# Performance work log

Hardware: AMD Instinct MI355X
Metric: run time of the kernel (lower is better)

Reference implementation:

```python
import jax, jax.numpy as jnp
import numpy as np

HARMONICS = 5


def _harmonic_basis(x):
    k = jnp.arange(1, HARMONICS + 1, dtype=x.dtype)            # [H]
    kx = x[..., None] * k                                       # [B, D, H]
    sc = jnp.stack([jnp.sin(kx), jnp.cos(kx)], axis=-1)         # [B, D, H, 2]
    sc = sc.reshape(*x.shape, 2 * HARMONICS)                    # interleaved sin/cos
    ones = jnp.ones((*x.shape, 1), dtype=x.dtype)
    return jnp.concatenate([ones, sc], axis=-1)                 # [B, D, 2H+1]


def setup_inputs() -> dict:
    key = jax.random.key(0)
    k1, k2, k3 = jax.random.split(key, 3)
    B, D, F, H = 16384, 256, 11, 256
    x = jax.random.normal(k1, (B, D), dtype=jnp.float32)
    W = jax.random.normal(k2, (D, F, H), dtype=jnp.float32) * (1.0 / np.sqrt(F))
    b = jax.random.normal(k3, (D, H), dtype=jnp.float32) * 0.01
    return {"x": x, "W": W, "b": b}


def reference(x, W, b) -> jnp.ndarray:
    # basis expansion per feature, batched small GEMM, summed over features
    basis = _harmonic_basis(x)                                  # [B, D, F]
    out = jnp.einsum('bdf,dfh->bh', basis, W)                   # sum over features fused
    out = out + jnp.sum(b, axis=0)                              # sum of per-feature biases
    return out
```

## Files before the change

kernel.cpp:

```cpp
#include <hip/hip_runtime.h>
#include <hip/hip_bf16.h>
#include <hip/hip_fp16.h>


#define BDIM 16384
#define DDIM 256
#define HOUT 256
#define NKT  80
#define BM 128
#define BN 128

typedef _Float16 halfx8 __attribute__((ext_vector_type(8)));
typedef float floatx4 __attribute__((ext_vector_type(4)));

__device__ __forceinline__ unsigned short f2h(float f) {
    union { _Float16 h; unsigned short u; } v;
    v.h = (_Float16)f;
    return v.u;
}

#define INV2PI 0.15915494309189535f

__device__ __forceinline__ void hwsincos(float x, float* s, float* c) {
    const float r = x * INV2PI;
    float sv, cv;
    asm("v_sin_f32 %0, %1" : "=v"(sv) : "v"(r));
    asm("v_cos_f32 %0, %1" : "=v"(cv) : "v"(r));
    *s = sv; *c = cv;
}

__global__ void prep_kernel(const float* __restrict__ W, const float* __restrict__ bias,
                            unsigned short* __restrict__ Wfrag, float* __restrict__ c_part) {
    const int bid = blockIdx.x;
    const int t = threadIdx.x;
    if (bid < 4 * NKT) {
        const int kt = bid >> 2;
        const int sub = bid & 3;
        const int dtile = kt / 10;
        const int f = kt - dtile * 10 + 1;
        const int d0 = dtile * 32 + sub * 8;
        const float* wsrc = W + ((size_t)d0 * 11 + f) * 256 + t;
        union { unsigned short s[8]; int4 v; } buf;
#pragma unroll
        for (int dd = 0; dd < 8; ++dd)
            buf.s[dd] = f2h(wsrc[(size_t)dd * 11 * 256]);
        *(int4*)(Wfrag + ((size_t)kt * 256 + t) * 32 + sub * 8) = buf.v;
    } else {
        const int p = bid - 4 * NKT;
        float acc = 0.f;
#pragma unroll
        for (int dd = 0; dd < 32; ++dd) {
            const int d = p * 32 + dd;
            acc += W[(size_t)(d * 11) * 256 + t] + bias[(size_t)d * 256 + t];
        }
        c_part[p * 256 + t] = acc;
    }
}

__global__ __launch_bounds__(512, 2)
void kan_gemm(const float* __restrict__ x, const unsigned short* __restrict__ Wfrag,
              const float* __restrict__ c_part, float* __restrict__ out) {
    __shared__ unsigned short Bs[6][2 * 8 * 512];

    const int t = threadIdx.x;
    const int m0 = blockIdx.x * BM;
    const int h0 = blockIdx.y * BN;

    const int lane = t & 63;
    const int wave = t >> 6;
    const int wr = wave >> 1;
    const int wc = wave & 1;
    const int l15 = lane & 15;
    const int koff = lane >> 4;

    floatx4 acc[2][4];
#pragma unroll
    for (int i = 0; i < 2; ++i)
#pragma unroll
        for (int j = 0; j < 4; ++j)
            acc[i][j] = (floatx4){0.f, 0.f, 0.f, 0.f};

    const float* xr0 = x + (size_t)(m0 + wr * 32 + l15) * DDIM + koff * 8;

    float4 xn[4];
    xn[0] = *(const float4*)(xr0 + 0);
    xn[1] = *(const float4*)(xr0 + 4);
    xn[2] = *(const float4*)(xr0 + 16 * DDIM + 0);
    xn[3] = *(const float4*)(xr0 + 16 * DDIM + 4);

#pragma unroll
    for (int p = 0; p < 3; ++p) {
#pragma unroll
        for (int s = 0; s < 2; ++s) {
            const int c = wave * 2 + s;
            const int ktl = c >> 3;
            const int f = c & 7;
            const unsigned short* g = Wfrag + (size_t)(p * 2 + ktl) * 8192
                                    + (h0 + f * 16 + l15) * 32 + koff * 8;
            __builtin_amdgcn_global_load_lds((const void*)g,
                (void*)(&Bs[p][0] + c * 512), 16, 0, 0);
        }
    }

    __half2 s1h[8], c1h[8], skh[8], ckh[8];

#pragma unroll 1
    for (int dt = 0; dt < 8; ++dt) {
#pragma unroll
        for (int q = 0; q < 5; ++q) {

            if (q == 2) {
                const int dn = (dt < 7) ? dt + 1 : 7;
                xn[0] = *(const float4*)(xr0 + dn * 32 + 0);
                xn[1] = *(const float4*)(xr0 + dn * 32 + 4);
                xn[2] = *(const float4*)(xr0 + 16 * DDIM + dn * 32 + 0);
                xn[3] = *(const float4*)(xr0 + 16 * DDIM + dn * 32 + 4);
            }

            {
                int pt = dt * 5 + q + 3;
                if (pt > 39) pt = 39;
#pragma unroll
                for (int s = 0; s < 2; ++s) {
                    const int c = wave * 2 + s;
                    const int ktl = c >> 3;
                    const int f = c & 7;
                    const unsigned short* g = Wfrag + (size_t)(pt * 2 + ktl) * 8192
                                            + (h0 + f * 16 + l15) * 32 + koff * 8;
                    __builtin_amdgcn_global_load_lds((const void*)g,
                        (void*)(&Bs[(q + 3) % 5][0] + c * 512), 16, 0, 0);
                }
            }

            __builtin_amdgcn_sched_barrier(0);
            if (q == 2 || q == 3) {
                asm volatile("s_waitcnt vmcnt(10)" ::: "memory");
            } else {
                asm volatile("s_waitcnt vmcnt(6)" ::: "memory");
            }
            __builtin_amdgcn_s_barrier();
            __builtin_amdgcn_sched_barrier(0);

            if (q == 0) {
                const float xv[16] = {xn[0].x, xn[0].y, xn[0].z, xn[0].w,
                                      xn[1].x, xn[1].y, xn[1].z, xn[1].w,
                                      xn[2].x, xn[2].y, xn[2].z, xn[2].w,
                                      xn[3].x, xn[3].y, xn[3].z, xn[3].w};
#pragma unroll
                for (int p = 0; p < 8; ++p) {
                    float s0, c0, s1, c1;
                    hwsincos(xv[2 * p], &s0, &c0);
                    hwsincos(xv[2 * p + 1], &s1, &c1);
                    const __half2 sh = __floats2half2_rn(s0, s1);
                    const __half2 ch = __floats2half2_rn(c0, c1);
                    s1h[p] = sh; c1h[p] = ch;
                    skh[p] = sh; ckh[p] = ch;
                }
            }

#pragma unroll
            for (int s = 0; s < 2; ++s) {
                union { __half2 h2[4]; halfx8 v; } a0, a1;
                if (s == 0) {
#pragma unroll
                    for (int p = 0; p < 4; ++p) { a0.h2[p] = skh[p]; a1.h2[p] = skh[p + 4]; }
                } else {
#pragma unroll
                    for (int p = 0; p < 4; ++p) { a0.h2[p] = ckh[p]; a1.h2[p] = ckh[p + 4]; }
                }

                const unsigned short* fb = &Bs[q][(s * 8 + wc * 4) * 512 + lane * 8];
                const halfx8 b0 = *(const halfx8*)(fb);
                const halfx8 b1 = *(const halfx8*)(fb + 512);
                const halfx8 b2 = *(const halfx8*)(fb + 1024);
                const halfx8 b3 = *(const halfx8*)(fb + 1536);

                acc[0][0] = __builtin_amdgcn_mfma_f32_16x16x32_f16(a0.v, b0, acc[0][0], 0, 0, 0);
                acc[1][0] = __builtin_amdgcn_mfma_f32_16x16x32_f16(a1.v, b0, acc[1][0], 0, 0, 0);
                acc[0][1] = __builtin_amdgcn_mfma_f32_16x16x32_f16(a0.v, b1, acc[0][1], 0, 0, 0);
                acc[1][1] = __builtin_amdgcn_mfma_f32_16x16x32_f16(a1.v, b1, acc[1][1], 0, 0, 0);
                acc[0][2] = __builtin_amdgcn_mfma_f32_16x16x32_f16(a0.v, b2, acc[0][2], 0, 0, 0);
                acc[1][2] = __builtin_amdgcn_mfma_f32_16x16x32_f16(a1.v, b2, acc[1][2], 0, 0, 0);
                acc[0][3] = __builtin_amdgcn_mfma_f32_16x16x32_f16(a0.v, b3, acc[0][3], 0, 0, 0);
                acc[1][3] = __builtin_amdgcn_mfma_f32_16x16x32_f16(a1.v, b3, acc[1][3], 0, 0, 0);

                if (s == 1 && q < 4) {
#pragma unroll
                    for (int p = 0; p < 8; ++p) {
                        const __half2 t0 = __hmul2(ckh[p], s1h[p]);
                        const __half2 t1 = __hmul2(skh[p], s1h[p]);
                        const __half2 ns = __hfma2(skh[p], c1h[p], t0);
                        const __half2 nc = __hfma2(ckh[p], c1h[p], __hneg2(t1));
                        skh[p] = ns;
                        ckh[p] = nc;
                    }
                }
            }
        }
    }

    asm volatile("s_waitcnt vmcnt(0)" ::: "memory");

    float cj[4];
#pragma unroll
    for (int j = 0; j < 4; ++j) {
        const int col = h0 + wc * 64 + j * 16 + l15;
        float s = 0.f;
#pragma unroll
        for (int q = 0; q < 8; ++q) s += c_part[q * 256 + col];
        cj[j] = s;
    }
#pragma unroll
    for (int i = 0; i < 2; ++i) {
        const int row0 = m0 + wr * 32 + i * 16 + koff * 4;
#pragma unroll
        for (int j = 0; j < 4; ++j) {
            const int col = h0 + wc * 64 + j * 16 + l15;
#pragma unroll
            for (int r = 0; r < 4; ++r)
                out[(size_t)(row0 + r) * HOUT + col] = acc[i][j][r] + cj[j];
        }
    }
}

extern "C" void kernel_launch(void* const* d_in, const int* in_sizes, int n_in,
                              void* d_out, int out_size, void* d_ws, size_t ws_size,
                              hipStream_t stream) {
    const float* x = (const float*)d_in[0];
    const float* W = (const float*)d_in[1];
    const float* b = (const float*)d_in[2];
    float* out = (float*)d_out;

    unsigned short* Wfrag = (unsigned short*)d_ws;
    float* c_part = (float*)((char*)d_ws + (size_t)NKT * 256 * 32 * 2);

    prep_kernel<<<4 * NKT + 8, 256, 0, stream>>>(W, b, Wfrag, c_part);
    kan_gemm<<<dim3(BDIM / BM, HOUT / BN), 512, 0, stream>>>(x, Wfrag, c_part, out);
}
```

Measured before the change: 97.24 us.

## Remap waves to 64x32 sub-tiles to cut LDS B-fragment reads

```diff
diff --git a/kernel.cpp b/kernel.cpp
--- a/kernel.cpp
+++ b/kernel.cpp
@@ -68,25 +68,26 @@
 
     const int lane = t & 63;
     const int wave = t >> 6;
-    const int wr = wave >> 1;
-    const int wc = wave & 1;
+    const int rg = wave >> 2;
+    const int cg = wave & 3;
     const int l15 = lane & 15;
     const int koff = lane >> 4;
 
-    floatx4 acc[2][4];
-#pragma unroll
-    for (int i = 0; i < 2; ++i)
-#pragma unroll
-        for (int j = 0; j < 4; ++j)
+    floatx4 acc[4][2];
+#pragma unroll
+    for (int i = 0; i < 4; ++i)
+#pragma unroll
+        for (int j = 0; j < 2; ++j)
             acc[i][j] = (floatx4){0.f, 0.f, 0.f, 0.f};
 
-    const float* xr0 = x + (size_t)(m0 + wr * 32 + l15) * DDIM + koff * 8;
-
-    float4 xn[4];
-    xn[0] = *(const float4*)(xr0 + 0);
-    xn[1] = *(const float4*)(xr0 + 4);
-    xn[2] = *(const float4*)(xr0 + 16 * DDIM + 0);
-    xn[3] = *(const float4*)(xr0 + 16 * DDIM + 4);
+    const float* xr0 = x + (size_t)(m0 + rg * 64 + l15) * DDIM + koff * 8;
+
+    float4 xn[8];
+#pragma unroll
+    for (int i = 0; i < 4; ++i) {
+        xn[2 * i]     = *(const float4*)(xr0 + (size_t)i * 16 * DDIM + 0);
+        xn[2 * i + 1] = *(const float4*)(xr0 + (size_t)i * 16 * DDIM + 4);
+    }
 
 #pragma unroll
     for (int p = 0; p < 3; ++p) {
@@ -102,7 +103,7 @@
         }
     }
 
-    __half2 s1h[8], c1h[8], skh[8], ckh[8];
+    __half2 s1h[16], c1h[16], skh[16], ckh[16];
 
 #pragma unroll 1
     for (int dt = 0; dt < 8; ++dt) {
@@ -111,10 +112,11 @@
 
             if (q == 2) {
                 const int dn = (dt < 7) ? dt + 1 : 7;
-                xn[0] = *(const float4*)(xr0 + dn * 32 + 0);
-                xn[1] = *(const float4*)(xr0 + dn * 32 + 4);
-                xn[2] = *(const float4*)(xr0 + 16 * DDIM + dn * 32 + 0);
-                xn[3] = *(const float4*)(xr0 + 16 * DDIM + dn * 32 + 4);
+#pragma unroll
+                for (int i = 0; i < 4; ++i) {
+                    xn[2 * i]     = *(const float4*)(xr0 + (size_t)i * 16 * DDIM + dn * 32 + 0);
+                    xn[2 * i + 1] = *(const float4*)(xr0 + (size_t)i * 16 * DDIM + dn * 32 + 4);
+                }
             }
 
             {
@@ -134,7 +136,7 @@
 
             __builtin_amdgcn_sched_barrier(0);
             if (q == 2 || q == 3) {
-                asm volatile("s_waitcnt vmcnt(10)" ::: "memory");
+                asm volatile("s_waitcnt vmcnt(14)" ::: "memory");
             } else {
                 asm volatile("s_waitcnt vmcnt(6)" ::: "memory");
             }
@@ -142,51 +144,51 @@
             __builtin_amdgcn_sched_barrier(0);
 
             if (q == 0) {
-                const float xv[16] = {xn[0].x, xn[0].y, xn[0].z, xn[0].w,
-                                      xn[1].x, xn[1].y, xn[1].z, xn[1].w,
-                                      xn[2].x, xn[2].y, xn[2].z, xn[2].w,
-                                      xn[3].x, xn[3].y, xn[3].z, xn[3].w};
-#pragma unroll
-                for (int p = 0; p < 8; ++p) {
-                    float s0, c0, s1, c1;
-                    hwsincos(xv[2 * p], &s0, &c0);
-                    hwsincos(xv[2 * p + 1], &s1, &c1);
-                    const __half2 sh = __floats2half2_rn(s0, s1);
-                    const __half2 ch = __floats2half2_rn(c0, c1);
-                    s1h[p] = sh; c1h[p] = ch;
-                    skh[p] = sh; ckh[p] = ch;
+#pragma unroll
+                for (int i = 0; i < 4; ++i) {
+                    const float xv[8] = {xn[2 * i].x, xn[2 * i].y, xn[2 * i].z, xn[2 * i].w,
+                                         xn[2 * i + 1].x, xn[2 * i + 1].y, xn[2 * i + 1].z, xn[2 * i + 1].w};
+#pragma unroll
+                    for (int pp = 0; pp < 4; ++pp) {
+                        float s0, c0, s1, c1;
+                        hwsincos(xv[2 * pp], &s0, &c0);
+                        hwsincos(xv[2 * pp + 1], &s1, &c1);
+                        const __half2 sh = __floats2half2_rn(s0, s1);
+                        const __half2 ch = __floats2half2_rn(c0, c1);
+                        s1h[i * 4 + pp] = sh; c1h[i * 4 + pp] = ch;
+                        skh[i * 4 + pp] = sh; ckh[i * 4 + pp] = ch;
+                    }
                 }
             }
 
 #pragma unroll
             for (int s = 0; s < 2; ++s) {
-                union { __half2 h2[4]; halfx8 v; } a0, a1;
+                union { __half2 h2[4]; halfx8 v; } a[4];
                 if (s == 0) {
 #pragma unroll
-                    for (int p = 0; p < 4; ++p) { a0.h2[p] = skh[p]; a1.h2[p] = skh[p + 4]; }
+                    for (int i = 0; i < 4; ++i)
+#pragma unroll
+                        for (int pp = 0; pp < 4; ++pp) a[i].h2[pp] = skh[i * 4 + pp];
                 } else {
 #pragma unroll
-                    for (int p = 0; p < 4; ++p) { a0.h2[p] = ckh[p]; a1.h2[p] = ckh[p + 4]; }
-                }
-
-                const unsigned short* fb = &Bs[q][(s * 8 + wc * 4) * 512 + lane * 8];
+                    for (int i = 0; i < 4; ++i)
+#pragma unroll
+                        for (int pp = 0; pp < 4; ++pp) a[i].h2[pp] = ckh[i * 4 + pp];
+                }
+
+                const unsigned short* fb = &Bs[q][(s * 8 + cg * 2) * 512 + lane * 8];
                 const halfx8 b0 = *(const halfx8*)(fb);
                 const halfx8 b1 = *(const halfx8*)(fb + 512);
-                const halfx8 b2 = *(const halfx8*)(fb + 1024);
-                const halfx8 b3 = *(const halfx8*)(fb + 1536);
-
-                acc[0][0] = __builtin_amdgcn_mfma_f32_16x16x32_f16(a0.v, b0, acc[0][0], 0, 0, 0);
-                acc[1][0] = __builtin_amdgcn_mfma_f32_16x16x32_f16(a1.v, b0, acc[1][0], 0, 0, 0);
-                acc[0][1] = __builtin_amdgcn_mfma_f32_16x16x32_f16(a0.v, b1, acc[0][1], 0, 0, 0);
-                acc[1][1] = __builtin_amdgcn_mfma_f32_16x16x32_f16(a1.v, b1, acc[1][1], 0, 0, 0);
-                acc[0][2] = __builtin_amdgcn_mfma_f32_16x16x32_f16(a0.v, b2, acc[0][2], 0, 0, 0);
-                acc[1][2] = __builtin_amdgcn_mfma_f32_16x16x32_f16(a1.v, b2, acc[1][2], 0, 0, 0);
-                acc[0][3] = __builtin_amdgcn_mfma_f32_16x16x32_f16(a0.v, b3, acc[0][3], 0, 0, 0);
-                acc[1][3] = __builtin_amdgcn_mfma_f32_16x16x32_f16(a1.v, b3, acc[1][3], 0, 0, 0);
+
+#pragma unroll
+                for (int i = 0; i < 4; ++i) {
+                    acc[i][0] = __builtin_amdgcn_mfma_f32_16x16x32_f16(a[i].v, b0, acc[i][0], 0, 0, 0);
+                    acc[i][1] = __builtin_amdgcn_mfma_f32_16x16x32_f16(a[i].v, b1, acc[i][1], 0, 0, 0);
+                }
 
                 if (s == 1 && q < 4) {
 #pragma unroll
-                    for (int p = 0; p < 8; ++p) {
+                    for (int p = 0; p < 16; ++p) {
                         const __half2 t0 = __hmul2(ckh[p], s1h[p]);
                         const __half2 t1 = __hmul2(skh[p], s1h[p]);
                         const __half2 ns = __hfma2(skh[p], c1h[p], t0);
@@ -201,21 +203,21 @@
 
     asm volatile("s_waitcnt vmcnt(0)" ::: "memory");
 
-    float cj[4];
-#pragma unroll
-    for (int j = 0; j < 4; ++j) {
-        const int col = h0 + wc * 64 + j * 16 + l15;
+    float cj[2];
+#pragma unroll
+    for (int j = 0; j < 2; ++j) {
+        const int col = h0 + cg * 32 + j * 16 + l15;
         float s = 0.f;
 #pragma unroll
         for (int q = 0; q < 8; ++q) s += c_part[q * 256 + col];
         cj[j] = s;
     }
 #pragma unroll
-    for (int i = 0; i < 2; ++i) {
-        const int row0 = m0 + wr * 32 + i * 16 + koff * 4;
-#pragma unroll
-        for (int j = 0; j < 4; ++j) {
-            const int col = h0 + wc * 64 + j * 16 + l15;
+    for (int i = 0; i < 4; ++i) {
+        const int row0 = m0 + rg * 64 + i * 16 + koff * 4;
+#pragma unroll
+        for (int j = 0; j < 2; ++j) {
+            const int col = h0 + cg * 32 + j * 16 + l15;
 #pragma unroll
             for (int r = 0; r < 4; ++r)
                 out[(size_t)(row0 + r) * HOUT + col] = acc[i][j][r] + cj[j];
```

After: 108.3 us. 11.4% more time.

## Restructure B-tile pipeline into 16 phases of 5 k-steps with triple buffering

Applied to the files above, without the earlier changes.

```diff
diff --git a/kernel.cpp b/kernel.cpp
--- a/kernel.cpp
+++ b/kernel.cpp
@@ -60,7 +60,7 @@
 __global__ __launch_bounds__(512, 2)
 void kan_gemm(const float* __restrict__ x, const unsigned short* __restrict__ Wfrag,
               const float* __restrict__ c_part, float* __restrict__ out) {
-    __shared__ unsigned short Bs[6][2 * 8 * 512];
+    __shared__ unsigned short Bs[3 * 20480];
 
     const int t = threadIdx.x;
     const int m0 = blockIdx.x * BM;
@@ -88,115 +88,118 @@
     xn[2] = *(const float4*)(xr0 + 16 * DDIM + 0);
     xn[3] = *(const float4*)(xr0 + 16 * DDIM + 4);
 
-#pragma unroll
-    for (int p = 0; p < 3; ++p) {
-#pragma unroll
-        for (int s = 0; s < 2; ++s) {
-            const int c = wave * 2 + s;
-            const int ktl = c >> 3;
-            const int f = c & 7;
-            const unsigned short* g = Wfrag + (size_t)(p * 2 + ktl) * 8192
-                                    + (h0 + f * 16 + l15) * 32 + koff * 8;
-            __builtin_amdgcn_global_load_lds((const void*)g,
-                (void*)(&Bs[p][0] + c * 512), 16, 0, 0);
-        }
+    unsigned short* cur = Bs;
+    unsigned short* nxt = Bs + 20480;
+    unsigned short* thr = Bs + 40960;
+
+#pragma unroll
+    for (int s = 0; s < 5; ++s) {
+        const int c = wave * 5 + s;
+        const int ktl = c >> 3;
+        const int f = c & 7;
+        const unsigned short* g = Wfrag + (size_t)ktl * 8192
+                                + (h0 + f * 16 + l15) * 32 + koff * 8;
+        __builtin_amdgcn_global_load_lds((const void*)g, (void*)(cur + c * 512), 16, 0, 0);
     }
 
     __half2 s1h[8], c1h[8], skh[8], ckh[8];
 
 #pragma unroll 1
-    for (int dt = 0; dt < 8; ++dt) {
-#pragma unroll
-        for (int q = 0; q < 5; ++q) {
-
-            if (q == 2) {
-                const int dn = (dt < 7) ? dt + 1 : 7;
-                xn[0] = *(const float4*)(xr0 + dn * 32 + 0);
-                xn[1] = *(const float4*)(xr0 + dn * 32 + 4);
-                xn[2] = *(const float4*)(xr0 + 16 * DDIM + dn * 32 + 0);
-                xn[3] = *(const float4*)(xr0 + 16 * DDIM + dn * 32 + 4);
-            }
-
-            {
-                int pt = dt * 5 + q + 3;
-                if (pt > 39) pt = 39;
-#pragma unroll
-                for (int s = 0; s < 2; ++s) {
-                    const int c = wave * 2 + s;
-                    const int ktl = c >> 3;
-                    const int f = c & 7;
-                    const unsigned short* g = Wfrag + (size_t)(pt * 2 + ktl) * 8192
-                                            + (h0 + f * 16 + l15) * 32 + koff * 8;
-                    __builtin_amdgcn_global_load_lds((const void*)g,
-                        (void*)(&Bs[(q + 3) % 5][0] + c * 512), 16, 0, 0);
+    for (int ph = 0; ph < 16; ++ph) {
+        const int dt = ph >> 1;
+        const int half = ph & 1;
+
+        {
+            int pt = ph + 1;
+            if (pt > 15) pt = 15;
+#pragma unroll
+            for (int s = 0; s < 5; ++s) {
+                const int c = wave * 5 + s;
+                const int ktl = c >> 3;
+                const int f = c & 7;
+                const unsigned short* g = Wfrag + (size_t)(pt * 5 + ktl) * 8192
+                                        + (h0 + f * 16 + l15) * 32 + koff * 8;
+                __builtin_amdgcn_global_load_lds((const void*)g, (void*)(nxt + c * 512), 16, 0, 0);
+            }
+        }
+
+        if (half == 1) {
+            const int dn = (dt < 7) ? dt + 1 : 7;
+            xn[0] = *(const float4*)(xr0 + dn * 32 + 0);
+            xn[1] = *(const float4*)(xr0 + dn * 32 + 4);
+            xn[2] = *(const float4*)(xr0 + 16 * DDIM + dn * 32 + 0);
+            xn[3] = *(const float4*)(xr0 + 16 * DDIM + dn * 32 + 4);
+        }
+
+        __builtin_amdgcn_sched_barrier(0);
+        if (half == 0) {
+            asm volatile("s_waitcnt vmcnt(5)" ::: "memory");
+        } else {
+            asm volatile("s_waitcnt vmcnt(9)" ::: "memory");
+        }
+        __builtin_amdgcn_s_barrier();
+        __builtin_amdgcn_sched_barrier(0);
+
+        if (half == 0) {
+#pragma unroll
+            for (int p = 0; p < 8; ++p) {
+                float s0, c0, s1, c1;
+                const float xv0 = ((const float*)&xn[p >> 1])[(p & 1) * 2];
+                const float xv1 = ((const float*)&xn[p >> 1])[(p & 1) * 2 + 1];
+                hwsincos(xv0, &s0, &c0);
+                hwsincos(xv1, &s1, &c1);
+                const __half2 sh = __floats2half2_rn(s0, s1);
+                const __half2 ch = __floats2half2_rn(c0, c1);
+                s1h[p] = sh; c1h[p] = ch;
+                skh[p] = sh; ckh[p] = ch;
+            }
+        }
+
+#pragma unroll
+        for (int kl = 0; kl < 5; ++kl) {
+            const int hs = half * 5 + kl;
+
+            union { __half2 h2[4]; halfx8 v; } a0, a1;
+            if (hs & 1) {
+#pragma unroll
+                for (int p = 0; p < 4; ++p) { a0.h2[p] = ckh[p]; a1.h2[p] = ckh[p + 4]; }
+            } else {
+#pragma unroll
+                for (int p = 0; p < 4; ++p) { a0.h2[p] = skh[p]; a1.h2[p] = skh[p + 4]; }
+            }
+
+            const unsigned short* fb = cur + (kl * 8 + wc * 4) * 512 + lane * 8;
+            const halfx8 b0 = *(const halfx8*)(fb);
+            const halfx8 b1 = *(const halfx8*)(fb + 512);
+            const halfx8 b2 = *(const halfx8*)(fb + 1024);
+            const halfx8 b3 = *(const halfx8*)(fb + 1536);
+
+            acc[0][0] = __builtin_amdgcn_mfma_f32_16x16x32_f16(a0.v, b0, acc[0][0], 0, 0, 0);
+            acc[1][0] = __builtin_amdgcn_mfma_f32_16x16x32_f16(a1.v, b0, acc[1][0], 0, 0, 0);
+            acc[0][1] = __builtin_amdgcn_mfma_f32_16x16x32_f16(a0.v, b1, acc[0][1], 0, 0, 0);
+            acc[1][1] = __builtin_amdgcn_mfma_f32_16x16x32_f16(a1.v, b1, acc[1][1], 0, 0, 0);
+            acc[0][2] = __builtin_amdgcn_mfma_f32_16x16x32_f16(a0.v, b2, acc[0][2], 0, 0, 0);
+            acc[1][2] = __builtin_amdgcn_mfma_f32_16x16x32_f16(a1.v, b2, acc[1][2], 0, 0, 0);
+            acc[0][3] = __builtin_amdgcn_mfma_f32_16x16x32_f16(a0.v, b3, acc[0][3], 0, 0, 0);
+            acc[1][3] = __builtin_amdgcn_mfma_f32_16x16x32_f16(a1.v, b3, acc[1][3], 0, 0, 0);
+
+            if ((hs & 1) && hs < 9) {
+#pragma unroll
+                for (int p = 0; p < 8; ++p) {
+                    const __half2 t0 = __hmul2(ckh[p], s1h[p]);
+                    const __half2 t1 = __hmul2(skh[p], s1h[p]);
+                    const __half2 ns = __hfma2(skh[p], c1h[p], t0);
+                    const __half2 nc = __hfma2(ckh[p], c1h[p], __hneg2(t1));
+                    skh[p] = ns;
+                    ckh[p] = nc;
                 }
             }
-
-            __builtin_amdgcn_sched_barrier(0);
-            if (q == 2 || q == 3) {
-                asm volatile("s_waitcnt vmcnt(10)" ::: "memory");
-            } else {
-                asm volatile("s_waitcnt vmcnt(6)" ::: "memory");
-            }
-            __builtin_amdgcn_s_barrier();
-            __builtin_amdgcn_sched_barrier(0);
-
-            if (q == 0) {
-                const float xv[16] = {xn[0].x, xn[0].y, xn[0].z, xn[0].w,
-                                      xn[1].x, xn[1].y, xn[1].z, xn[1].w,
-                                      xn[2].x, xn[2].y, xn[2].z, xn[2].w,
-                                      xn[3].x, xn[3].y, xn[3].z, xn[3].w};
-#pragma unroll
-                for (int p = 0; p < 8; ++p) {
-                    float s0, c0, s1, c1;
-                    hwsincos(xv[2 * p], &s0, &c0);
-                    hwsincos(xv[2 * p + 1], &s1, &c1);
-                    const __half2 sh = __floats2half2_rn(s0, s1);
-                    const __half2 ch = __floats2half2_rn(c0, c1);
-                    s1h[p] = sh; c1h[p] = ch;
-                    skh[p] = sh; ckh[p] = ch;
-                }
-            }
-
-#pragma unroll
-            for (int s = 0; s < 2; ++s) {
-                union { __half2 h2[4]; halfx8 v; } a0, a1;
-                if (s == 0) {
-#pragma unroll
-                    for (int p = 0; p < 4; ++p) { a0.h2[p] = skh[p]; a1.h2[p] = skh[p + 4]; }
-                } else {
-#pragma unroll
-                    for (int p = 0; p < 4; ++p) { a0.h2[p] = ckh[p]; a1.h2[p] = ckh[p + 4]; }
-                }
-
-                const unsigned short* fb = &Bs[q][(s * 8 + wc * 4) * 512 + lane * 8];
-                const halfx8 b0 = *(const halfx8*)(fb);
-                const halfx8 b1 = *(const halfx8*)(fb + 512);
-                const halfx8 b2 = *(const halfx8*)(fb + 1024);
-                const halfx8 b3 = *(const halfx8*)(fb + 1536);
-
-                acc[0][0] = __builtin_amdgcn_mfma_f32_16x16x32_f16(a0.v, b0, acc[0][0], 0, 0, 0);
-                acc[1][0] = __builtin_amdgcn_mfma_f32_16x16x32_f16(a1.v, b0, acc[1][0], 0, 0, 0);
-                acc[0][1] = __builtin_amdgcn_mfma_f32_16x16x32_f16(a0.v, b1, acc[0][1], 0, 0, 0);
-                acc[1][1] = __builtin_amdgcn_mfma_f32_16x16x32_f16(a1.v, b1, acc[1][1], 0, 0, 0);
-                acc[0][2] = __builtin_amdgcn_mfma_f32_16x16x32_f16(a0.v, b2, acc[0][2], 0, 0, 0);
-                acc[1][2] = __builtin_amdgcn_mfma_f32_16x16x32_f16(a1.v, b2, acc[1][2], 0, 0, 0);
-                acc[0][3] = __builtin_amdgcn_mfma_f32_16x16x32_f16(a0.v, b3, acc[0][3], 0, 0, 0);
-                acc[1][3] = __builtin_amdgcn_mfma_f32_16x16x32_f16(a1.v, b3, acc[1][3], 0, 0, 0);
-
-                if (s == 1 && q < 4) {
-#pragma unroll
-                    for (int p = 0; p < 8; ++p) {
-                        const __half2 t0 = __hmul2(ckh[p], s1h[p]);
-                        const __half2 t1 = __hmul2(skh[p], s1h[p]);
-                        const __half2 ns = __hfma2(skh[p], c1h[p], t0);
-                        const __half2 nc = __hfma2(ckh[p], c1h[p], __hneg2(t1));
-                        skh[p] = ns;
-                        ckh[p] = nc;
-                    }
-                }
-            }
-        }
+        }
+
+        unsigned short* tmp = cur;
+        cur = nxt;
+        nxt = thr;
+        thr = tmp;
     }
 
     asm volatile("s_waitcnt vmcnt(0)" ::: "memory");
```

Measured after the change: 100.9 us. 3.8% more time.
